# Kernel tuning notes

Measured on AMD Instinct MI355X. Metric: run time of the kernel, lower is better.

## Reference

```python
import jax, jax.numpy as jnp
import numpy as np

INV_TEMP = 10.0
_LOG_2PI = float(np.log(2.0 * np.pi))


def log_vmf_norm_const(kappa, dim):
    """log C_dim(kappa) = (dim/2-1)*log(kappa) - (dim/2)*log(2*pi) - log I_{dim/2-1}(kappa),
    with log I_v(kappa) via the uniform asymptotic expansion (as used in mkirchhof/url)."""
    v = dim / 2.0 - 1.0
    s = jnp.sqrt(v * v + kappa * kappa)
    log_iv = s + v * jnp.log(kappa / (v + s)) - 0.5 * _LOG_2PI - 0.25 * jnp.log(v * v + kappa * kappa)
    return v * jnp.log(kappa) - (dim / 2.0) * _LOG_2PI - log_iv


def _normalize(x, eps=1e-12):
    # matches torch F.normalize: x / max(||x||, eps)
    n = jnp.linalg.norm(x, axis=-1, keepdims=True)
    return x / jnp.maximum(n, eps)


def setup_inputs() -> dict:
    key = jax.random.key(0)
    kf, ku, ky, kw, kp = jax.random.split(key, 5)
    B, C, D = 2048, 16384, 128
    features = jax.random.normal(kf, (B, D), jnp.float32)
    unc = jax.random.uniform(ku, (B,), jnp.float32, minval=0.05, maxval=1.0)
    y = jax.random.randint(ky, (B,), 0, C)
    classifier_weight = jax.random.normal(kw, (C, D), jnp.float32)
    pred = jax.random.normal(kp, (B, C), jnp.float32)  # unused by the loss, kept for signature fidelity
    return {"pred": pred, "unc": unc, "y": y, "features": features,
            "classifier_weight": classifier_weight}


def reference(pred, unc, y, features, classifier_weight):
    dim = features.shape[-1]
    class_mu = _normalize(classifier_weight)                                  # [C, D]
    class_kappa = jnp.maximum(jnp.linalg.norm(classifier_weight, axis=-1), 1.0) * INV_TEMP  # [C]
    batch_mu = _normalize(features)                                           # [B, D]
    batch_kappa = 1.0 / unc                                                   # [B]

    # ||k1*mu1 + k2*mu2|| with unit mu's  ==  sqrt(k1^2 + k2^2 + 2*k1*k2*<mu1,mu2>)
    # (avoids the torch code's [B, C, D] broadcast; same math)
    dots = jnp.einsum('bd,cd->bc', batch_mu, class_mu)                        # [B, C]
    k1 = batch_kappa[:, None]                                                 # [B, 1]
    k2 = class_kappa[None, :]                                                 # [1, C]
    kappa3 = jnp.sqrt(jnp.maximum(k1 * k1 + k2 * k2 + 2.0 * k1 * k2 * dots, 1e-12))  # [B, C]

    sim = (log_vmf_norm_const(k1, dim) + log_vmf_norm_const(k2, dim)
           - log_vmf_norm_const(kappa3, dim))                                 # [B, C]

    gathered = jnp.take_along_axis(sim, y[:, None], axis=1)[:, 0]             # [B]
    lse = jax.nn.logsumexp(sim, axis=1)                                       # [B]
    return jnp.mean(-gathered + lse)
```

## Files before the change

### kernel.cpp

```cpp
#include <hip/hip_runtime.h>
#include <hip/hip_bf16.h>


typedef __bf16 bf16;
typedef __attribute__((ext_vector_type(8))) __bf16 bf16x8;
typedef __attribute__((ext_vector_type(4))) float f32x4;
typedef __attribute__((ext_vector_type(2))) float f32x2;

#define LOG2E 1.44269504088896340736f
#define LN2   0.69314718055994530942f
#define VNU   63.0f
#define VSQ   3969.0f

#if __has_builtin(__builtin_amdgcn_exp2f)
#define EXP2F(x) __builtin_amdgcn_exp2f(x)
#else
#define EXP2F(x) exp2f(x)
#endif
#if __has_builtin(__builtin_amdgcn_sqrtf)
#define SQRTF(x) __builtin_amdgcn_sqrtf(x)
#else
#define SQRTF(x) sqrtf(x)
#endif
#if __has_builtin(__builtin_amdgcn_logf)
#define LOG2F(x) __builtin_amdgcn_logf(x)
#else
#define LOG2F(x) __log2f(x)
#endif

#define QC0  289.4379f
#define QC1  -48.9193f
#define QC2  -2.9400f
#define QC3  0.51653f
#define QC4  -0.11373f

__global__ __launch_bounds__(256) void vmf_prepF(
    const float* __restrict__ feat, const float* __restrict__ unc,
    bf16* __restrict__ swF, float* __restrict__ k1,
    float* __restrict__ sumrow, int B)
{
  const int lane = threadIdx.x & 63;
  const int b    = blockIdx.x * 4 + (threadIdx.x >> 6);
  if (b >= B) return;
  float2 xv = reinterpret_cast<const float2*>(feat + (size_t)b * 128)[lane];
  float ssq = fmaf(xv.x, xv.x, xv.y * xv.y);
  #pragma unroll
  for (int off = 32; off; off >>= 1) ssq += __shfl_xor(ssq, off);
  float inv = 1.0f / fmaxf(sqrtf(ssq), 1e-12f);
  __hip_bfloat162 hv = __float22bfloat162_rn(make_float2(xv.x * inv, xv.y * inv));
  const int t   = b >> 4;
  const int l15 = b & 15;
  const int kk  = lane >> 4;
  const int qq  = (lane >> 2) & 3;
  const int j   = 2 * (lane & 3);
  const size_t eoff = (((size_t)(t * 4 + kk)) * 64 + qq * 16 + l15) * 8 + j;
  *reinterpret_cast<__hip_bfloat162*>(swF + eoff) = hv;
  if (lane == 0) k1[b] = 1.0f / unc[b];
  if (lane == 1) sumrow[b] = 0.0f;
}

__global__ __launch_bounds__(256, 4) void vmf_main(
    const float* __restrict__ W, const bf16* __restrict__ swF,
    const float* __restrict__ k1a, const int* __restrict__ y,
    float* __restrict__ sumrow, float* __restrict__ g2, int B, int NR)
{
  __shared__ bf16  ldsA[4][2048];
  __shared__ float4 ldsC[64];
  __shared__ float ldsSum[512];

  const int lane = threadIdx.x & 63;
  const int wave = threadIdx.x >> 6;
  const int q    = lane >> 4;
  const int l15  = lane & 15;
  const int bx   = blockIdx.x;

  {
    const int r16 = lane >> 2;
    const int p   = lane & 3;
    const int gc  = bx * 64 + wave * 16 + r16;
    const float4* wp = reinterpret_cast<const float4*>(W + (size_t)gc * 128 + p * 32);
    float4 xv[8];
    float ssq = 0.f;
    #pragma unroll
    for (int i = 0; i < 8; ++i) {
      xv[i] = wp[i];
      ssq += xv[i].x * xv[i].x + xv[i].y * xv[i].y +
             xv[i].z * xv[i].z + xv[i].w * xv[i].w;
    }
    ssq += __shfl_xor(ssq, 1);
    ssq += __shfl_xor(ssq, 2);
    float norm = sqrtf(ssq);
    float inv  = 1.0f / fmaxf(norm, 1e-12f);
    #pragma unroll
    for (int q2 = 0; q2 < 4; ++q2) {
      float4 a = xv[2 * q2], c = xv[2 * q2 + 1];
      __hip_bfloat162 h[4] = {
        __float22bfloat162_rn(make_float2(a.x * inv, a.y * inv)),
        __float22bfloat162_rn(make_float2(a.z * inv, a.w * inv)),
        __float22bfloat162_rn(make_float2(c.x * inv, c.y * inv)),
        __float22bfloat162_rn(make_float2(c.z * inv, c.w * inv))};
      *reinterpret_cast<bf16x8*>(&ldsA[wave][(p * 64 + q2 * 16 + r16) * 8]) =
          *reinterpret_cast<bf16x8*>(h);
    }
    if (p == 0) {
      float kap = fmaxf(norm, 1.0f) * 10.0f;
      float s2  = sqrtf(fmaf(kap, kap, VSQ));
      float f2l = fmaf(VNU, LOG2F(VNU + s2), 0.5f * LOG2F(s2)) - LOG2E * s2;
      ldsC[wave * 16 + r16] = make_float4(2.0f * kap, fmaf(kap, kap, VSQ), f2l, 0.0f);
    }
  }
  for (int i = threadIdx.x; i < NR; i += 256) ldsSum[i] = 0.f;
  __syncthreads();

  bf16x8 af[4];
  #pragma unroll
  for (int kk = 0; kk < 4; ++kk)
    af[kk] = *reinterpret_cast<bf16x8*>(&ldsA[wave][(kk * 64 + lane) * 8]);
  f32x2 cvx[4], cvy[4], cvz[4];
  int cls_lo[4];
  #pragma unroll
  for (int r = 0; r < 4; ++r) {
    float4 c = ldsC[wave * 16 + q * 4 + r];
    cvx[r] = (f32x2){c.x, c.x};
    cvy[r] = (f32x2){c.y, c.y};
    cvz[r] = (f32x2){c.z, c.z};
    cls_lo[r] = bx * 64 + wave * 16 + q * 4 + r;
  }

  const int rowbase = blockIdx.y * NR;
  const int nchunk  = NR / 32;
  int rt = rowbase >> 4;
  bf16x8 bfr[2][4];
  #pragma unroll
  for (int tl = 0; tl < 2; ++tl)
    #pragma unroll
    for (int kk = 0; kk < 4; ++kk)
      bfr[tl][kk] = *reinterpret_cast<const bf16x8*>(
          swF + (((size_t)(rt + tl) * 4 + kk) * 64 + lane) * 8);

  for (int ch = 0; ch < nchunk; ++ch) {
    const int row0 = rowbase + ch * 32 + l15;
    const int row1 = row0 + 16;
    const float k10 = k1a[row0], k11 = k1a[row1];
    const int   yv0 = y[row0],   yv1 = y[row1];
    const f32x2 k1pk   = {k10, k11};
    const f32x2 k1sqpk = k1pk * k1pk;

    bf16x8 bfn[2][4];
    if (ch + 1 < nchunk) {
      const int tn = rt + 2;
      #pragma unroll
      for (int tl = 0; tl < 2; ++tl)
        #pragma unroll
        for (int kk = 0; kk < 4; ++kk)
          bfn[tl][kk] = *reinterpret_cast<const bf16x8*>(
              swF + (((size_t)(tn + tl) * 4 + kk) * 64 + lane) * 8);
    }

    f32x4 acc0 = {0.f, 0.f, 0.f, 0.f};
    f32x4 acc1 = {0.f, 0.f, 0.f, 0.f};
    #pragma unroll
    for (int kk = 0; kk < 4; ++kk) {
      acc0 = __builtin_amdgcn_mfma_f32_16x16x32_bf16(af[kk], bfr[0][kk], acc0, 0, 0, 0);
      acc1 = __builtin_amdgcn_mfma_f32_16x16x32_bf16(af[kk], bfr[1][kk], acc1, 0, 0, 0);
    }

    f32x2 z[4];
    f32x2 sum = {0.f, 0.f};
    #pragma unroll
    for (int r = 0; r < 4; ++r) {
      f32x2 acc2 = {acc0[r], acc1[r]};
      f32x2 u = __builtin_elementwise_fma(cvx[r] * k1pk, acc2, k1sqpk + cvy[r]);
      u = __builtin_elementwise_max(u, (f32x2){VSQ, VSQ});
      f32x2 s3 = {SQRTF(u.x), SQRTF(u.y)};
      f32x2 t  = __builtin_elementwise_fma((f32x2){0.02f, 0.02f}, s3,
                                           (f32x2){-2.7f, -2.7f});
      f32x2 p  = __builtin_elementwise_fma(t, (f32x2){QC4, QC4}, (f32x2){QC3, QC3});
      p = __builtin_elementwise_fma(t, p, (f32x2){QC2, QC2});
      p = __builtin_elementwise_fma(t, p, (f32x2){QC1, QC1});
      p = __builtin_elementwise_fma(t, p, (f32x2){QC0, QC0});
      z[r] = cvz[r] - p;
      sum += (f32x2){EXP2F(z[r].x), EXP2F(z[r].y)};
    }
    if ((yv0 >> 2) == (cls_lo[0] >> 2)) {
      int rr = yv0 - cls_lo[0];
      float zz = rr == 0 ? z[0].x : rr == 1 ? z[1].x : rr == 2 ? z[2].x : z[3].x;
      g2[row0] = zz;
    }
    if ((yv1 >> 2) == (cls_lo[0] >> 2)) {
      int rr = yv1 - cls_lo[0];
      float zz = rr == 0 ? z[0].y : rr == 1 ? z[1].y : rr == 2 ? z[2].y : z[3].y;
      g2[row1] = zz;
    }
    sum.x += __shfl_xor(sum.x, 16); sum.x += __shfl_xor(sum.x, 32);
    sum.y += __shfl_xor(sum.y, 16); sum.y += __shfl_xor(sum.y, 32);
    if (q == 0) {
      atomicAdd(&ldsSum[ch * 32 + l15], sum.x);
      atomicAdd(&ldsSum[ch * 32 + 16 + l15], sum.y);
    }
    #pragma unroll
    for (int tl = 0; tl < 2; ++tl)
      #pragma unroll
      for (int kk = 0; kk < 4; ++kk) bfr[tl][kk] = bfn[tl][kk];
    rt += 2;
  }

  __syncthreads();
  for (int i = threadIdx.x; i < NR; i += 256)
    atomicAdd(&sumrow[rowbase + i], ldsSum[i]);
}

__global__ __launch_bounds__(1024) void vmf_finish(
    const float* __restrict__ sumrow, const float* __restrict__ g2,
    float* __restrict__ out, int B)
{
  float acc = 0.f;
  for (int b = threadIdx.x; b < B; b += 1024)
    acc += LN2 * (LOG2F(sumrow[b]) - g2[b]);
  #pragma unroll
  for (int off = 32; off; off >>= 1) acc += __shfl_down(acc, off);
  __shared__ float red[16];
  if ((threadIdx.x & 63) == 0) red[threadIdx.x >> 6] = acc;
  __syncthreads();
  if (threadIdx.x < 16) {
    float v = red[threadIdx.x];
    v += __shfl_down(v, 8);
    v += __shfl_down(v, 4);
    v += __shfl_down(v, 2);
    v += __shfl_down(v, 1);
    if (threadIdx.x == 0) out[0] = v / (float)B;
  }
}

extern "C" void kernel_launch(void* const* d_in, const int* in_sizes, int n_in,
                              void* d_out, int out_size, void* d_ws, size_t ws_size,
                              hipStream_t stream)
{
  const float* unc  = (const float*)d_in[1];
  const int*   yin  = (const int*)d_in[2];
  const float* feat = (const float*)d_in[3];
  const float* W    = (const float*)d_in[4];
  const int B = in_sizes[1];
  const int D = 128;
  const int C = in_sizes[4] / D;
  const int YS = 4;
  const int NR = B / YS;

  char* ws = (char*)d_ws;
  size_t off = 0;
  auto alloc = [&](size_t bytes) -> void* {
    void* p = ws + off;
    off += (bytes + 255) & ~(size_t)255;
    return p;
  };
  bf16*  swF    = (bf16*)alloc((size_t)B * D * sizeof(bf16));
  float* k1v    = (float*)alloc((size_t)B * 4);
  float* g2     = (float*)alloc((size_t)B * 4);
  float* sumrow = (float*)alloc((size_t)B * 4);

  vmf_prepF<<<(B + 3) / 4, 256, 0, stream>>>(feat, unc, swF, k1v, sumrow, B);
  dim3 g1(C / 64, YS);
  vmf_main<<<g1, 256, 0, stream>>>(W, swF, k1v, yin, sumrow, g2, B, NR);
  vmf_finish<<<1, 1024, 0, stream>>>(sumrow, g2, (float*)d_out, B);
}
```

Measured before the change: 206.4 us.

## Replace LDS and global atomics with per-wave partial sums and parallel finish

The main kernel no longer accumulates row sums through LDS atomics and a block-end global atomic flush. Each wave now writes its per-row partial exp-sum into a large partial buffer, and a 128-block finish kernel reduces the partials and atomically adds into the output. It also prefetches k1 and y one chunk ahead, hardcodes the loop trip count and unrolls by two. The cost is an 8 MB partial-buffer write and re-read in exchange for removing atomic contention and the trailing syncthreads.

```diff
diff --git a/kernel.cpp b/kernel.cpp
--- a/kernel.cpp
+++ b/kernel.cpp
@@ -37,8 +37,9 @@
 __global__ __launch_bounds__(256) void vmf_prepF(
     const float* __restrict__ feat, const float* __restrict__ unc,
     bf16* __restrict__ swF, float* __restrict__ k1,
-    float* __restrict__ sumrow, int B)
-{
+    float* __restrict__ out0, int B)
+{
+  if (blockIdx.x == 0 && threadIdx.x == 0) out0[0] = 0.0f;
   const int lane = threadIdx.x & 63;
   const int b    = blockIdx.x * 4 + (threadIdx.x >> 6);
   if (b >= B) return;
@@ -56,17 +57,15 @@
   const size_t eoff = (((size_t)(t * 4 + kk)) * 64 + qq * 16 + l15) * 8 + j;
   *reinterpret_cast<__hip_bfloat162*>(swF + eoff) = hv;
   if (lane == 0) k1[b] = 1.0f / unc[b];
-  if (lane == 1) sumrow[b] = 0.0f;
 }
 
 __global__ __launch_bounds__(256, 4) void vmf_main(
     const float* __restrict__ W, const bf16* __restrict__ swF,
-    const float* __restrict__ k1a, const int* __restrict__ y,
-    float* __restrict__ sumrow, float* __restrict__ g2, int B, int NR)
-{
-  __shared__ bf16  ldsA[4][2048];
+    const float* __restrict__ k1a, const int* __restrict__ yy,
+    float* __restrict__ partial, float* __restrict__ g2)
+{
+  __shared__ bf16   ldsA[4][2048];
   __shared__ float4 ldsC[64];
-  __shared__ float ldsSum[512];
 
   const int lane = threadIdx.x & 63;
   const int wave = threadIdx.x >> 6;
@@ -109,45 +108,41 @@
       ldsC[wave * 16 + r16] = make_float4(2.0f * kap, fmaf(kap, kap, VSQ), f2l, 0.0f);
     }
   }
-  for (int i = threadIdx.x; i < NR; i += 256) ldsSum[i] = 0.f;
   __syncthreads();
 
   bf16x8 af[4];
   #pragma unroll
   for (int kk = 0; kk < 4; ++kk)
     af[kk] = *reinterpret_cast<bf16x8*>(&ldsA[wave][(kk * 64 + lane) * 8]);
+  const int cls_base = bx * 64 + wave * 16 + q * 4;
   f32x2 cvx[4], cvy[4], cvz[4];
-  int cls_lo[4];
   #pragma unroll
   for (int r = 0; r < 4; ++r) {
     float4 c = ldsC[wave * 16 + q * 4 + r];
     cvx[r] = (f32x2){c.x, c.x};
     cvy[r] = (f32x2){c.y, c.y};
     cvz[r] = (f32x2){c.z, c.z};
-    cls_lo[r] = bx * 64 + wave * 16 + q * 4 + r;
-  }
-
-  const int rowbase = blockIdx.y * NR;
-  const int nchunk  = NR / 32;
+  }
+
+  const int rowbase = (int)blockIdx.y << 9;
+  const int pbase   = (bx * 4 + wave) * 2048;
   int rt = rowbase >> 4;
-  bf16x8 bfr[2][4];
+  bf16x8 bfr[2][4], bfn[2][4];
   #pragma unroll
   for (int tl = 0; tl < 2; ++tl)
     #pragma unroll
     for (int kk = 0; kk < 4; ++kk)
       bfr[tl][kk] = *reinterpret_cast<const bf16x8*>(
           swF + (((size_t)(rt + tl) * 4 + kk) * 64 + lane) * 8);
-
-  for (int ch = 0; ch < nchunk; ++ch) {
+  float k10 = k1a[rowbase + l15], k11 = k1a[rowbase + 16 + l15];
+  int   yv0 = yy[rowbase + l15],  yv1 = yy[rowbase + 16 + l15];
+
+  #pragma unroll 2
+  for (int ch = 0; ch < 16; ++ch) {
     const int row0 = rowbase + ch * 32 + l15;
-    const int row1 = row0 + 16;
-    const float k10 = k1a[row0], k11 = k1a[row1];
-    const int   yv0 = y[row0],   yv1 = y[row1];
-    const f32x2 k1pk   = {k10, k11};
-    const f32x2 k1sqpk = k1pk * k1pk;
-
-    bf16x8 bfn[2][4];
-    if (ch + 1 < nchunk) {
+    float k10n = 0.f, k11n = 0.f;
+    int   yv0n = 0,   yv1n = 0;
+    if (ch + 1 < 16) {
       const int tn = rt + 2;
       #pragma unroll
       for (int tl = 0; tl < 2; ++tl)
@@ -155,6 +150,8 @@
         for (int kk = 0; kk < 4; ++kk)
           bfn[tl][kk] = *reinterpret_cast<const bf16x8*>(
               swF + (((size_t)(tn + tl) * 4 + kk) * 64 + lane) * 8);
+      k10n = k1a[row0 + 32]; k11n = k1a[row0 + 48];
+      yv0n = yy[row0 + 32];  yv1n = yy[row0 + 48];
     }
 
     f32x4 acc0 = {0.f, 0.f, 0.f, 0.f};
@@ -165,6 +162,8 @@
       acc1 = __builtin_amdgcn_mfma_f32_16x16x32_bf16(af[kk], bfr[1][kk], acc1, 0, 0, 0);
     }
 
+    const f32x2 k1pk   = {k10, k11};
+    const f32x2 k1sqpk = k1pk * k1pk;
     f32x2 z[4];
     f32x2 sum = {0.f, 0.f};
     #pragma unroll
@@ -182,53 +181,56 @@
       z[r] = cvz[r] - p;
       sum += (f32x2){EXP2F(z[r].x), EXP2F(z[r].y)};
     }
-    if ((yv0 >> 2) == (cls_lo[0] >> 2)) {
-      int rr = yv0 - cls_lo[0];
+    if ((yv0 & ~3) == cls_base) {
+      int rr = yv0 - cls_base;
       float zz = rr == 0 ? z[0].x : rr == 1 ? z[1].x : rr == 2 ? z[2].x : z[3].x;
       g2[row0] = zz;
     }
-    if ((yv1 >> 2) == (cls_lo[0] >> 2)) {
-      int rr = yv1 - cls_lo[0];
+    if ((yv1 & ~3) == cls_base) {
+      int rr = yv1 - cls_base;
       float zz = rr == 0 ? z[0].y : rr == 1 ? z[1].y : rr == 2 ? z[2].y : z[3].y;
-      g2[row1] = zz;
+      g2[row0 + 16] = zz;
     }
     sum.x += __shfl_xor(sum.x, 16); sum.x += __shfl_xor(sum.x, 32);
     sum.y += __shfl_xor(sum.y, 16); sum.y += __shfl_xor(sum.y, 32);
     if (q == 0) {
-      atomicAdd(&ldsSum[ch * 32 + l15], sum.x);
-      atomicAdd(&ldsSum[ch * 32 + 16 + l15], sum.y);
+      partial[pbase + row0]      = sum.x;
+      partial[pbase + row0 + 16] = sum.y;
     }
     #pragma unroll
     for (int tl = 0; tl < 2; ++tl)
       #pragma unroll
       for (int kk = 0; kk < 4; ++kk) bfr[tl][kk] = bfn[tl][kk];
+    k10 = k10n; k11 = k11n; yv0 = yv0n; yv1 = yv1n;
     rt += 2;
   }
-
+}
+
+__global__ __launch_bounds__(256) void vmf_finish(
+    const float* __restrict__ partial, const float* __restrict__ g2,
+    float* __restrict__ out)
+{
+  const int tid = threadIdx.x;
+  const int jt  = tid & 15;
+  const int rl  = tid >> 4;
+  const int row = blockIdx.x * 16 + rl;
+  float s = 0.f;
+  #pragma unroll 8
+  for (int i = 0; i < 64; ++i)
+    s += partial[(size_t)(jt + 16 * i) * 2048 + row];
+  s += __shfl_xor(s, 1);
+  s += __shfl_xor(s, 2);
+  s += __shfl_xor(s, 4);
+  s += __shfl_xor(s, 8);
+  float contrib = (jt == 0) ? LN2 * (LOG2F(s) - g2[row]) : 0.f;
+  contrib += __shfl_xor(contrib, 16);
+  contrib += __shfl_xor(contrib, 32);
+  __shared__ float red[4];
+  if ((tid & 63) == 0) red[tid >> 6] = contrib;
   __syncthreads();
-  for (int i = threadIdx.x; i < NR; i += 256)
-    atomicAdd(&sumrow[rowbase + i], ldsSum[i]);
-}
-
-__global__ __launch_bounds__(1024) void vmf_finish(
-    const float* __restrict__ sumrow, const float* __restrict__ g2,
-    float* __restrict__ out, int B)
-{
-  float acc = 0.f;
-  for (int b = threadIdx.x; b < B; b += 1024)
-    acc += LN2 * (LOG2F(sumrow[b]) - g2[b]);
-  #pragma unroll
-  for (int off = 32; off; off >>= 1) acc += __shfl_down(acc, off);
-  __shared__ float red[16];
-  if ((threadIdx.x & 63) == 0) red[threadIdx.x >> 6] = acc;
-  __syncthreads();
-  if (threadIdx.x < 16) {
-    float v = red[threadIdx.x];
-    v += __shfl_down(v, 8);
-    v += __shfl_down(v, 4);
-    v += __shfl_down(v, 2);
-    v += __shfl_down(v, 1);
-    if (threadIdx.x == 0) out[0] = v / (float)B;
+  if (tid == 0) {
+    float blocksum = red[0] + red[1] + red[2] + red[3];
+    atomicAdd(out, blocksum * (1.0f / 2048.0f));
   }
 }
 
@@ -243,8 +245,6 @@
   const int B = in_sizes[1];
   const int D = 128;
   const int C = in_sizes[4] / D;
-  const int YS = 4;
-  const int NR = B / YS;
 
   char* ws = (char*)d_ws;
   size_t off = 0;
@@ -253,13 +253,14 @@
     off += (bytes + 255) & ~(size_t)255;
     return p;
   };
-  bf16*  swF    = (bf16*)alloc((size_t)B * D * sizeof(bf16));
-  float* k1v    = (float*)alloc((size_t)B * 4);
-  float* g2     = (float*)alloc((size_t)B * 4);
-  float* sumrow = (float*)alloc((size_t)B * 4);
-
-  vmf_prepF<<<(B + 3) / 4, 256, 0, stream>>>(feat, unc, swF, k1v, sumrow, B);
-  dim3 g1(C / 64, YS);
-  vmf_main<<<g1, 256, 0, stream>>>(W, swF, k1v, yin, sumrow, g2, B, NR);
-  vmf_finish<<<1, 1024, 0, stream>>>(sumrow, g2, (float*)d_out, B);
-}
+  bf16*  swF     = (bf16*)alloc((size_t)B * D * sizeof(bf16));
+  float* k1v     = (float*)alloc((size_t)B * 4);
+  float* g2      = (float*)alloc((size_t)B * 4);
+  float* partial = (float*)alloc((size_t)1024 * 2048 * 4);
+
+  vmf_prepF<<<(B + 3) / 4, 256, 0, stream>>>(feat, unc, swF, k1v,
+                                             (float*)d_out, B);
+  dim3 g1(C / 64, 4);
+  vmf_main<<<g1, 256, 0, stream>>>(W, swF, k1v, yin, partial, g2);
+  vmf_finish<<<128, 256, 0, stream>>>(partial, g2, (float*)d_out);
+}
```

Measured after the change: 213.2 us. 3.3% more time.
